# Kernel tuning notes

Measured on AMD Instinct MI355X. Metric: run time of the kernel, lower is better.

The kernel has to match this reference:

```python
import jax, jax.numpy as jnp
import numpy as np

N = 50000
E = 1600000
EP = 500000
D_IN, D_EMB = 64, 32


def setup_inputs() -> dict:
    key = jax.random.key(0)
    ks = jax.random.split(key, 12)
    return {
        "x": jax.random.normal(ks[0], (N, D_IN), dtype=jnp.float32),
        "W1": jax.random.normal(ks[1], (D_IN, D_EMB), dtype=jnp.float32) * (1.0 / np.sqrt(D_IN)),
        "b1": jnp.zeros((D_EMB,), dtype=jnp.float32),
        "W2": jax.random.normal(ks[2], (D_EMB, 2 * D_EMB), dtype=jnp.float32) * (1.0 / np.sqrt(D_EMB)),
        "b2": jnp.zeros((2 * D_EMB,), dtype=jnp.float32),
        "eps": jax.random.normal(ks[3], (N, D_EMB), dtype=jnp.float32),
        "edge_src": jax.random.randint(ks[4], (E,), 0, N, dtype=jnp.int32),
        "edge_dst": jax.random.randint(ks[5], (E,), 0, N, dtype=jnp.int32),
        "pos_src": jax.random.randint(ks[6], (EP,), 0, N, dtype=jnp.int32),
        "pos_dst": jax.random.randint(ks[7], (EP,), 0, N, dtype=jnp.int32),
        "neg_src": jax.random.randint(ks[8], (EP,), 0, N, dtype=jnp.int32),
        "neg_dst": jax.random.randint(ks[9], (EP,), 0, N, dtype=jnp.int32),
    }


def _degree_norms(src, dst, n):
    ones = jnp.ones(src.shape, dtype=jnp.float32)
    out_deg = jax.ops.segment_sum(ones, src, num_segments=n)
    in_deg = jax.ops.segment_sum(ones, dst, num_segments=n)
    # DGL GraphConv norm='both': clamp degrees to >=1, pow(-0.5)
    return jnp.clip(out_deg, 1.0) ** -0.5, jnp.clip(in_deg, 1.0) ** -0.5


def _graph_conv(h, src, dst, norm_src, norm_dst, W, b, n):
    # rst = D_dst^{-1/2} A D_src^{-1/2} h W + b
    msg = (h * norm_src[:, None])[src]                       # [E, d] gather
    agg = jax.ops.segment_sum(msg, dst, num_segments=n)      # [N, d] scatter-add
    return (agg * norm_dst[:, None]) @ W + b


def _dot_predict(z, u, v):
    # u_dot_v: per-edge inner product of endpoint embeddings
    return jnp.sum(z[u] * z[v], axis=-1)


def reference(x, W1, b1, W2, b2, eps, edge_src, edge_dst,
              pos_src, pos_dst, neg_src, neg_dst):
    n = x.shape[0]
    ns, nd = _degree_norms(edge_src, edge_dst, n)
    h = _graph_conv(x, edge_src, edge_dst, ns, nd, W1, b1, n)
    h = jax.nn.relu(h)  # dropout = identity (eval mode)
    h = _graph_conv(h, edge_src, edge_dst, ns, nd, W2, b2, n)
    mu, log_var = jnp.split(h, 2, axis=-1)
    sigma = jnp.exp(log_var / 2.0)
    z = mu + sigma * eps
    pos = _dot_predict(z, pos_src, pos_dst)
    neg = _dot_predict(z, neg_src, neg_dst)
    return pos, neg, mu, sigma
```

## Files before the change

### kernel.cpp

```cpp
#include <hip/hip_runtime.h>
#include <math.h>

#define NN  50000
#define NE  1600000
#define NEP 500000
#define DIN 64
#define DE  32

#define BKT_SH 7
#define NB     391
#define S1B    256
#define CHK    6250
#define HBS    128
#define HCHKS  12500
#define HWRD   12500
#define HWRD2  12512
#define XWB    3126
#define CAP    6144
#define NROW   50016

typedef float f4 __attribute__((ext_vector_type(4)));

__device__ __forceinline__ unsigned f2b(float f) {
    unsigned u = __float_as_uint(f);
    return (u + 0x7FFFu + ((u >> 16) & 1u)) >> 16;
}
__device__ __forceinline__ unsigned pack2(float a, float b) {
    return f2b(a) | (f2b(b) << 16);
}
__device__ __forceinline__ float blo(unsigned u) { return __uint_as_float(u << 16); }
__device__ __forceinline__ float bhi(unsigned u) { return __uint_as_float(u & 0xFFFF0000u); }

__global__ __launch_bounds__(256) void k_hist(const int* __restrict__ src,
                                              const int* __restrict__ dst,
                                              unsigned* __restrict__ partialS,
                                              unsigned* __restrict__ partialD,
                                              int* __restrict__ T) {
    __shared__ unsigned h[HWRD2];
    int t = threadIdx.x;
    int isS = blockIdx.x < HBS;
    int chunk = isS ? blockIdx.x : blockIdx.x - HBS;
    const int* e = isS ? src : dst;
    int chk = isS ? HCHKS : CHK;
    for (int i = t; i < HWRD2; i += 256) h[i] = 0;
    __syncthreads();
    int beg = chunk * chk;
    const int ev = beg + chk;
    int i = beg + t;
    for (; i + 1792 < ev; i += 2048) {
        int s0 = e[i],        s1 = e[i + 256],  s2 = e[i + 512],  s3 = e[i + 768];
        int s4 = e[i + 1024], s5 = e[i + 1280], s6 = e[i + 1536], s7 = e[i + 1792];
        atomicAdd(&h[s0 >> 2], 1u << ((s0 & 3) * 8));
        atomicAdd(&h[s1 >> 2], 1u << ((s1 & 3) * 8));
        atomicAdd(&h[s2 >> 2], 1u << ((s2 & 3) * 8));
        atomicAdd(&h[s3 >> 2], 1u << ((s3 & 3) * 8));
        atomicAdd(&h[s4 >> 2], 1u << ((s4 & 3) * 8));
        atomicAdd(&h[s5 >> 2], 1u << ((s5 & 3) * 8));
        atomicAdd(&h[s6 >> 2], 1u << ((s6 & 3) * 8));
        atomicAdd(&h[s7 >> 2], 1u << ((s7 & 3) * 8));
    }
    for (; i < ev; i += 256) {
        int s = e[i];
        atomicAdd(&h[s >> 2], 1u << ((s & 3) * 8));
    }
    __syncthreads();
    unsigned* pout = (isS ? partialS : partialD) + (size_t)chunk * HWRD;
    for (int i2 = t; i2 < HWRD; i2 += 256) pout[i2] = h[i2];
    if (!isS) {
        for (int c = t; c < NB; c += 256) {
            int sum = 0;
#pragma unroll
            for (int k = 0; k < 32; k++) {
                unsigned v = h[c * 32 + ((k + t) & 31)];
                sum += (int)(v & 0xFFu) + (int)((v >> 8) & 0xFFu)
                     + (int)((v >> 16) & 0xFFu) + (int)(v >> 24);
            }
            T[chunk * NB + c] = sum;
        }
    }
}

__global__ __launch_bounds__(512) void k_s2h(const int* __restrict__ T,
                                             int* __restrict__ Base,
                                             int* __restrict__ BS,
                                             const unsigned* __restrict__ partialS,
                                             const unsigned* __restrict__ partialD,
                                             int* __restrict__ dout,
                                             int* __restrict__ din) {
    int t = threadIdx.x;
    if (blockIdx.x == 0) {
        __shared__ int tot[512];
        int run = 0;
        if (t < NB) {
            for (int b = 0; b < S1B; b += 8) {
                int v0 = T[(b + 0) * NB + t];
                int v1 = T[(b + 1) * NB + t];
                int v2 = T[(b + 2) * NB + t];
                int v3 = T[(b + 3) * NB + t];
                int v4 = T[(b + 4) * NB + t];
                int v5 = T[(b + 5) * NB + t];
                int v6 = T[(b + 6) * NB + t];
                int v7 = T[(b + 7) * NB + t];
                Base[(b + 0) * NB + t] = run; run += v0;
                Base[(b + 1) * NB + t] = run; run += v1;
                Base[(b + 2) * NB + t] = run; run += v2;
                Base[(b + 3) * NB + t] = run; run += v3;
                Base[(b + 4) * NB + t] = run; run += v4;
                Base[(b + 5) * NB + t] = run; run += v5;
                Base[(b + 6) * NB + t] = run; run += v6;
                Base[(b + 7) * NB + t] = run; run += v7;
            }
        }
        tot[t] = (t < NB) ? run : 0;
        __syncthreads();
        for (int off = 1; off < 512; off <<= 1) {
            int v = (t >= off) ? tot[t - off] : 0;
            __syncthreads();
            tot[t] += v;
            __syncthreads();
        }
        if (t < NB) BS[t] = (t == 0) ? 0 : tot[t - 1];
        if (t == 0) BS[NB] = NE;
    } else if (blockIdx.x < 26) {
        int w = (blockIdx.x - 1) * 512 + t;
        if (w < HWRD) {
            int c0 = 0, c1 = 0, c2 = 0, c3 = 0;
#pragma unroll 8
            for (int b = 0; b < HBS; b++) {
                unsigned v = partialS[(size_t)b * HWRD + w];
                c0 += (int)(v & 0xFFu);
                c1 += (int)((v >> 8) & 0xFFu);
                c2 += (int)((v >> 16) & 0xFFu);
                c3 += (int)(v >> 24);
            }
            ((int4*)dout)[w] = make_int4(c0, c1, c2, c3);
        }
    } else {
        int w = (blockIdx.x - 26) * 512 + t;
        if (w < HWRD) {
            int c0 = 0, c1 = 0, c2 = 0, c3 = 0;
#pragma unroll 8
            for (int b = 0; b < S1B; b++) {
                unsigned v = partialD[(size_t)b * HWRD + w];
                c0 += (int)(v & 0xFFu);
                c1 += (int)((v >> 8) & 0xFFu);
                c2 += (int)((v >> 16) & 0xFFu);
                c3 += (int)(v >> 24);
            }
            ((int4*)din)[w] = make_int4(c0, c1, c2, c3);
        }
    }
}

__global__ __launch_bounds__(512) void k_s3(const int* __restrict__ src,
                                            const int* __restrict__ dst,
                                            const int* __restrict__ T,
                                            const int* __restrict__ Base,
                                            const int* __restrict__ BS,
                                            unsigned* __restrict__ tmp) {
    __shared__ int scn[512];
    __shared__ int delta[NB];
    __shared__ int cur[NB];
    __shared__ unsigned buf[CHK];
    int t = threadIdx.x;
    int beg = blockIdx.x * CHK;
    scn[t] = (t < NB) ? T[blockIdx.x * NB + t] : 0;
    __syncthreads();
    for (int off = 1; off < 512; off <<= 1) {
        int v = (t >= off) ? scn[t - off] : 0;
        __syncthreads();
        scn[t] += v;
        __syncthreads();
    }
    if (t < NB) {
        int ls = (t == 0) ? 0 : scn[t - 1];
        cur[t] = ls;
        delta[t] = Base[blockIdx.x * NB + t] + BS[t] - ls;
    }
    __syncthreads();
    {
        const int ev = beg + CHK;
        int i = beg + t;
        for (; i + 1536 < ev; i += 2048) {
            int d0 = dst[i],        s0 = src[i];
            int d1 = dst[i + 512],  s1 = src[i + 512];
            int d2 = dst[i + 1024], s2 = src[i + 1024];
            int d3 = dst[i + 1536], s3 = src[i + 1536];
            int l0 = atomicAdd(&cur[d0 >> BKT_SH], 1); buf[l0] = (unsigned)s0 | ((unsigned)d0 << 16);
            int l1 = atomicAdd(&cur[d1 >> BKT_SH], 1); buf[l1] = (unsigned)s1 | ((unsigned)d1 << 16);
            int l2 = atomicAdd(&cur[d2 >> BKT_SH], 1); buf[l2] = (unsigned)s2 | ((unsigned)d2 << 16);
            int l3 = atomicAdd(&cur[d3 >> BKT_SH], 1); buf[l3] = (unsigned)s3 | ((unsigned)d3 << 16);
        }
        for (; i < ev; i += 512) {
            int d = dst[i];
            int s = src[i];
            int lp = atomicAdd(&cur[d >> BKT_SH], 1);
            buf[lp] = (unsigned)s | ((unsigned)d << 16);
        }
    }
    __syncthreads();
    for (int i = t; i < CHK; i += 512) {
        unsigned e = buf[i];
        tmp[delta[e >> (16 + BKT_SH)] + i] = e;
    }
}

__global__ __launch_bounds__(256) void k_s4x(const unsigned* __restrict__ tmp,
                                             const int* __restrict__ BS,
                                             const int* __restrict__ din,
                                             ushort* __restrict__ csr,
                                             unsigned* __restrict__ prow,
                                             const float* __restrict__ x,
                                             const float* __restrict__ W1,
                                             const int* __restrict__ dout,
                                             unsigned* __restrict__ xw1b) {
    __shared__ float sW[DIN * DE];
    int t = threadIdx.x;
    if (blockIdx.x < NB) {
        int* scn = (int*)sW;
        int* cur = scn + 128;
        int p = blockIdx.x;
        int ebeg = BS[p];
        int ne = BS[p + 1] - ebeg;
        int myd = 0;
        if (t < 128) {
            int node = (p << BKT_SH) + t;
            myd = (node < NN) ? din[node] : 0;
            scn[t] = (myd + 7) & ~7;
        }
        __syncthreads();
        for (int off = 1; off < 128; off <<= 1) {
            int v = 0;
            if (t < 128 && t >= off) v = scn[t - off];
            __syncthreads();
            if (t < 128) scn[t] += v;
            __syncthreads();
        }
        if (t < 128) {
            int ps = p * CAP + scn[t] - ((myd + 7) & ~7);
            cur[t] = ps;
            int node = (p << BKT_SH) + t;
            if (node < NN) prow[node] = (unsigned)ps | ((unsigned)myd << 24);
        }
        __syncthreads();
        {
            int i = t;
            for (; i + 768 < ne; i += 1024) {
                unsigned e0 = tmp[ebeg + i];
                unsigned e1 = tmp[ebeg + i + 256];
                unsigned e2 = tmp[ebeg + i + 512];
                unsigned e3 = tmp[ebeg + i + 768];
                int l0 = atomicAdd(&cur[(e0 >> 16) & 127], 1); csr[l0] = (ushort)(e0 & 0xFFFFu);
                int l1 = atomicAdd(&cur[(e1 >> 16) & 127], 1); csr[l1] = (ushort)(e1 & 0xFFFFu);
                int l2 = atomicAdd(&cur[(e2 >> 16) & 127], 1); csr[l2] = (ushort)(e2 & 0xFFFFu);
                int l3 = atomicAdd(&cur[(e3 >> 16) & 127], 1); csr[l3] = (ushort)(e3 & 0xFFFFu);
            }
            for (; i < ne; i += 256) {
                unsigned e = tmp[ebeg + i];
                int lp = atomicAdd(&cur[(e >> 16) & 127], 1);
                csr[lp] = (ushort)(e & 0xFFFFu);
            }
        }
        __syncthreads();
        if (t < 128) {
            int end = p * CAP + scn[t];
            for (int q = cur[t]; q < end; q++) csr[q] = (ushort)NN;
        }
    } else {
        for (int i = t; i < DIN * DE; i += 256) sW[i] = W1[i];
        __syncthreads();
        int r  = (blockIdx.x - NB) * 16 + (t >> 4);
        int tc = t & 15;
        if (r >= NN) {
            if (r < NROW) xw1b[r * 16 + tc] = 0u;
            return;
        }
        const float* xr = x + (size_t)r * DIN;
        float a0 = 0.f, a1 = 0.f;
#pragma unroll
        for (int k = 0; k < DIN; k++) {
            float v = xr[k];
            a0 += v * sW[k * DE + 2 * tc];
            a1 += v * sW[k * DE + 2 * tc + 1];
        }
        float ns = rsqrtf(fmaxf((float)dout[r], 1.0f));
        xw1b[r * 16 + tc] = pack2(a0 * ns, a1 * ns);
    }
}

__device__ __forceinline__ void acc8(float* a, uint4 w) {
    a[0] += blo(w.x); a[1] += bhi(w.x);
    a[2] += blo(w.y); a[3] += bhi(w.y);
    a[4] += blo(w.z); a[5] += bhi(w.z);
    a[6] += blo(w.w); a[7] += bhi(w.w);
}

__device__ __forceinline__ void gacc(const uint4* __restrict__ msg, uint4 cw, int l, float* a) {
    uint4 w0 = msg[(int)(cw.x & 0xFFFFu) * 4 + l];
    uint4 w1 = msg[(int)(cw.x >> 16)     * 4 + l];
    uint4 w2 = msg[(int)(cw.y & 0xFFFFu) * 4 + l];
    uint4 w3 = msg[(int)(cw.y >> 16)     * 4 + l];
    uint4 w4 = msg[(int)(cw.z & 0xFFFFu) * 4 + l];
    uint4 w5 = msg[(int)(cw.z >> 16)     * 4 + l];
    uint4 w6 = msg[(int)(cw.w & 0xFFFFu) * 4 + l];
    uint4 w7 = msg[(int)(cw.w >> 16)     * 4 + l];
    acc8(a, w0); acc8(a, w1); acc8(a, w2); acc8(a, w3);
    acc8(a, w4); acc8(a, w5); acc8(a, w6); acc8(a, w7);
}

__device__ __forceinline__ void gather_half(const ushort* __restrict__ crow,
                                            const uint4* __restrict__ msg,
                                            int nb, int h, int l, float* a) {
    const uint4* cp = (const uint4*)crow;
    int b = h;
    if (b >= nb) return;
    uint4 cur = cp[b];
    for (b += 2; b < nb; b += 2) {
        uint4 nxt = cp[b];
        gacc(msg, cur, l, a);
        cur = nxt;
    }
    gacc(msg, cur, l, a);
}

__global__ __launch_bounds__(256) void k_g1(const unsigned* __restrict__ prow,
                                            const ushort* __restrict__ csr,
                                            const uint4* __restrict__ msg,
                                            const int* __restrict__ dout,
                                            const float* __restrict__ b1,
                                            uint4* __restrict__ out) {
    int t = blockIdx.x * 256 + threadIdx.x;
    int r = t >> 3;
    int l = t & 3;
    int h = (t >> 2) & 1;
    if (r >= NN) {
        if (h == 0 && r < NROW) out[r * 4 + l] = make_uint4(0, 0, 0, 0);
        return;
    }
    unsigned pr = prow[r];
    int ps = (int)(pr & 0xFFFFFFu);
    int len = (int)(pr >> 24);
    int nb = (len + 7) >> 3;
    float a[8] = {0, 0, 0, 0, 0, 0, 0, 0};
    gather_half(csr + ps, msg, nb, h, l, a);
#pragma unroll
    for (int k = 0; k < 8; k++) a[k] += __shfl_xor(a[k], 4);
    if (h) return;
    float scd = rsqrtf(fmaxf((float)len, 1.0f));
    float scs = rsqrtf(fmaxf((float)dout[r], 1.0f));
    const float4* b14 = (const float4*)b1;
    float4 bb0 = b14[2 * l], bb1 = b14[2 * l + 1];
    float o0 = fmaxf(scd * a[0] + bb0.x, 0.f) * scs;
    float o1 = fmaxf(scd * a[1] + bb0.y, 0.f) * scs;
    float o2 = fmaxf(scd * a[2] + bb0.z, 0.f) * scs;
    float o3 = fmaxf(scd * a[3] + bb0.w, 0.f) * scs;
    float o4 = fmaxf(scd * a[4] + bb1.x, 0.f) * scs;
    float o5 = fmaxf(scd * a[5] + bb1.y, 0.f) * scs;
    float o6 = fmaxf(scd * a[6] + bb1.z, 0.f) * scs;
    float o7 = fmaxf(scd * a[7] + bb1.w, 0.f) * scs;
    out[r * 4 + l] = make_uint4(pack2(o0, o1), pack2(o2, o3), pack2(o4, o5), pack2(o6, o7));
}

__global__ __launch_bounds__(256) void k_g2f(const unsigned* __restrict__ prow,
                                             const ushort* __restrict__ csr,
                                             const uint4* __restrict__ msg,
                                             const float* __restrict__ W2,
                                             const float* __restrict__ b2,
                                             const float* __restrict__ eps,
                                             float* __restrict__ mu,
                                             float* __restrict__ sigma,
                                             unsigned* __restrict__ zb) {
    __shared__ float sW[DE * 64];
    __shared__ float sb[64];
    int t = threadIdx.x;
    for (int i = t; i < DE * 64; i += 256) sW[i] = W2[i];
    if (t < 64) sb[t] = b2[t];
    __syncthreads();
    int g = blockIdx.x * 256 + t;
    int r = g >> 3;
    int l = g & 3;
    int j = g & 7;
    int h = (g >> 2) & 1;
    if (r >= NN) return;
    unsigned pr = prow[r];
    int ps = (int)(pr & 0xFFFFFFu);
    int len = (int)(pr >> 24);
    int nb = (len + 7) >> 3;
    float a[8] = {0, 0, 0, 0, 0, 0, 0, 0};
    gather_half(csr + ps, msg, nb, h, l, a);
#pragma unroll
    for (int k = 0; k < 8; k++) a[k] += __shfl_xor(a[k], 4);
    float scd = rsqrtf(fmaxf((float)len, 1.0f));
#pragma unroll
    for (int k = 0; k < 8; k++) a[k] *= scd;
    int cbase = 8 * j;
    float o3[8];
#pragma unroll
    for (int c = 0; c < 8; c++) o3[c] = sb[cbase + c];
#pragma unroll
    for (int d = 0; d < 4; d++) {
        int kb = 8 * (l ^ d);
#pragma unroll
        for (int k = 0; k < 8; k++) {
            float av = (d == 0) ? a[k] : __shfl_xor(a[k], d);
            const float* wrow = sW + (kb + k) * 64 + cbase;
#pragma unroll
            for (int c = 0; c < 8; c++) o3[c] += av * wrow[c];
        }
    }
    if (j < 4) {
        f4* mp = (f4*)(mu + (size_t)r * DE + cbase);
        f4 m0 = {o3[0], o3[1], o3[2], o3[3]};
        f4 m1 = {o3[4], o3[5], o3[6], o3[7]};
        __builtin_nontemporal_store(m0, mp);
        __builtin_nontemporal_store(m1, mp + 1);
    }
    float muv[8];
#pragma unroll
    for (int c = 0; c < 8; c++) muv[c] = __shfl_xor(o3[c], 4);
    if (j >= 4) {
        int cc = cbase - DE;
        const f4* ep = (const f4*)(eps + (size_t)r * DE + cc);
        f4 e0 = __builtin_nontemporal_load(ep);
        f4 e1 = __builtin_nontemporal_load(ep + 1);
        float ev[8] = {e0.x, e0.y, e0.z, e0.w, e1.x, e1.y, e1.z, e1.w};
        float sgv[8], zv[8];
#pragma unroll
        for (int c = 0; c < 8; c++) {
            sgv[c] = expf(0.5f * o3[c]);
            zv[c]  = muv[c] + sgv[c] * ev[c];
        }
        f4* sp = (f4*)(sigma + (size_t)r * DE + cc);
        f4 s0 = {sgv[0], sgv[1], sgv[2], sgv[3]};
        f4 s1 = {sgv[4], sgv[5], sgv[6], sgv[7]};
        __builtin_nontemporal_store(s0, sp);
        __builtin_nontemporal_store(s1, sp + 1);
        uint4* zp = (uint4*)(zb + (size_t)r * 16 + (j - 4) * 4);
        zp[0] = make_uint4(pack2(zv[0], zv[1]), pack2(zv[2], zv[3]),
                           pack2(zv[4], zv[5]), pack2(zv[6], zv[7]));
    }
}

__global__ __launch_bounds__(256) void k_dot2(const uint4* __restrict__ zb4,
                                              const int* __restrict__ pu,
                                              const int* __restrict__ pv,
                                              const int* __restrict__ nu,
                                              const int* __restrict__ nv,
                                              float* __restrict__ out) {
    int t = blockIdx.x * 256 + threadIdx.x;
    int e = t >> 2;
    int l = t & 3;
    if (e < 2 * NEP) {
        int ee = (e < NEP) ? e : e - NEP;
        const int* uu = (e < NEP) ? pu : nu;
        const int* vv = (e < NEP) ? pv : nv;
        int a = __builtin_nontemporal_load(uu + ee);
        int b = __builtin_nontemporal_load(vv + ee);
        uint4 za = zb4[a * 4 + l];
        uint4 zc = zb4[b * 4 + l];
        float s = blo(za.x) * blo(zc.x) + bhi(za.x) * bhi(zc.x)
                + blo(za.y) * blo(zc.y) + bhi(za.y) * bhi(zc.y)
                + blo(za.z) * blo(zc.z) + bhi(za.z) * bhi(zc.z)
                + blo(za.w) * blo(zc.w) + bhi(za.w) * bhi(zc.w);
        s += __shfl_xor(s, 1);
        s += __shfl_xor(s, 2);
        if (l == 0) __builtin_nontemporal_store(s, out + e);
    }
}

extern "C" void kernel_launch(void* const* d_in, const int* in_sizes, int n_in,
                              void* d_out, int out_size, void* d_ws, size_t ws_size,
                              hipStream_t stream) {
    const float* x    = (const float*)d_in[0];
    const float* W1   = (const float*)d_in[1];
    const float* b1   = (const float*)d_in[2];
    const float* W2   = (const float*)d_in[3];
    const float* b2   = (const float*)d_in[4];
    const float* eps  = (const float*)d_in[5];
    const int*   esrc = (const int*)d_in[6];
    const int*   edst = (const int*)d_in[7];
    const int*   psrc = (const int*)d_in[8];
    const int*   pdst = (const int*)d_in[9];
    const int*   gsrc = (const int*)d_in[10];
    const int*   gdst = (const int*)d_in[11];

    float* out = (float*)d_out;
    float* pos = out;
    float* mu  = out + 2 * NEP;
    float* sg  = out + 2 * NEP + NN * DE;

    int* wi = (int*)d_ws;
    unsigned* prow     = (unsigned*)wi;
    int*      dout_    = wi + 50004;
    int*      din      = wi + 100004;
    int*      T        = wi + 150004;
    int*      Base     = wi + 250100;
    int*      BS       = wi + 350196;
    unsigned* partialS = (unsigned*)(wi + 350592);
    unsigned* tmp      = partialS;
    unsigned* partialD = (unsigned*)(wi + 1950592);
    ushort*   csr      = (ushort*)partialD;
    unsigned* P0       = (unsigned*)(wi + 5150592);
    unsigned* P1       = P0 + 16 * NROW;

    k_hist<<<HBS + S1B, 256, 0, stream>>>(esrc, edst, partialS, partialD, T);
    k_s2h <<<51, 512, 0, stream>>>(T, Base, BS, partialS, partialD, dout_, din);
    k_s3  <<<S1B, 512, 0, stream>>>(esrc, edst, T, Base, BS, tmp);
    k_s4x <<<NB + XWB, 256, 0, stream>>>(tmp, BS, din, csr, prow, x, W1, dout_, P0);
    k_g1  <<<(NROW * 8) / 256, 256, 0, stream>>>(prow, csr, (const uint4*)P0, dout_, b1, (uint4*)P1);
    k_g2f <<<(NN * 8 + 255) / 256, 256, 0, stream>>>(prow, csr, (const uint4*)P1, W2, b2, eps, mu, sg, P0);
    k_dot2<<<(2 * NEP * 4) / 256, 256, 0, stream>>>((const uint4*)P0, psrc, pdst, gsrc, gdst, pos);
}
```

Before: 191.9 us.

## Derive in-degrees from bucketed edges instead of a full destination histogram

The per-node destination histogram (partialD, 256 blocks × 12500 words) and its reduction are removed. Destination blocks now count only per-bucket totals, and each bucket block in k_s4x recounts per-node in-degrees from the bucket-sorted tmp array in shared memory before building its CSR. This cuts a large partial-histogram write and read plus the extra reduction blocks, at the cost of one more pass over tmp per bucket. Block sizes are also doubled across k_hist, k_s3 and k_s4x.

```diff
diff --git a/kernel.cpp b/kernel.cpp
--- a/kernel.cpp
+++ b/kernel.cpp
@@ -14,8 +14,7 @@
 #define HBS    128
 #define HCHKS  12500
 #define HWRD   12500
-#define HWRD2  12512
-#define XWB    3126
+#define XWB    1563
 #define CAP    6144
 #define NROW   50016
 
@@ -31,52 +30,61 @@
 __device__ __forceinline__ float blo(unsigned u) { return __uint_as_float(u << 16); }
 __device__ __forceinline__ float bhi(unsigned u) { return __uint_as_float(u & 0xFFFF0000u); }
 
-__global__ __launch_bounds__(256) void k_hist(const int* __restrict__ src,
+__global__ __launch_bounds__(512) void k_hist(const int* __restrict__ src,
                                               const int* __restrict__ dst,
                                               unsigned* __restrict__ partialS,
-                                              unsigned* __restrict__ partialD,
                                               int* __restrict__ T) {
-    __shared__ unsigned h[HWRD2];
+    __shared__ unsigned h[HWRD];
     int t = threadIdx.x;
-    int isS = blockIdx.x < HBS;
-    int chunk = isS ? blockIdx.x : blockIdx.x - HBS;
-    const int* e = isS ? src : dst;
-    int chk = isS ? HCHKS : CHK;
-    for (int i = t; i < HWRD2; i += 256) h[i] = 0;
-    __syncthreads();
-    int beg = chunk * chk;
-    const int ev = beg + chk;
-    int i = beg + t;
-    for (; i + 1792 < ev; i += 2048) {
-        int s0 = e[i],        s1 = e[i + 256],  s2 = e[i + 512],  s3 = e[i + 768];
-        int s4 = e[i + 1024], s5 = e[i + 1280], s6 = e[i + 1536], s7 = e[i + 1792];
-        atomicAdd(&h[s0 >> 2], 1u << ((s0 & 3) * 8));
-        atomicAdd(&h[s1 >> 2], 1u << ((s1 & 3) * 8));
-        atomicAdd(&h[s2 >> 2], 1u << ((s2 & 3) * 8));
-        atomicAdd(&h[s3 >> 2], 1u << ((s3 & 3) * 8));
-        atomicAdd(&h[s4 >> 2], 1u << ((s4 & 3) * 8));
-        atomicAdd(&h[s5 >> 2], 1u << ((s5 & 3) * 8));
-        atomicAdd(&h[s6 >> 2], 1u << ((s6 & 3) * 8));
-        atomicAdd(&h[s7 >> 2], 1u << ((s7 & 3) * 8));
-    }
-    for (; i < ev; i += 256) {
-        int s = e[i];
-        atomicAdd(&h[s >> 2], 1u << ((s & 3) * 8));
-    }
-    __syncthreads();
-    unsigned* pout = (isS ? partialS : partialD) + (size_t)chunk * HWRD;
-    for (int i2 = t; i2 < HWRD; i2 += 256) pout[i2] = h[i2];
-    if (!isS) {
-        for (int c = t; c < NB; c += 256) {
-            int sum = 0;
-#pragma unroll
-            for (int k = 0; k < 32; k++) {
-                unsigned v = h[c * 32 + ((k + t) & 31)];
-                sum += (int)(v & 0xFFu) + (int)((v >> 8) & 0xFFu)
-                     + (int)((v >> 16) & 0xFFu) + (int)(v >> 24);
-            }
-            T[chunk * NB + c] = sum;
-        }
+    if (blockIdx.x < HBS) {
+        for (int i = t; i < HWRD; i += 512) h[i] = 0;
+        __syncthreads();
+        int beg = blockIdx.x * HCHKS;
+        const int ev = beg + HCHKS;
+        int i = beg + t;
+        for (; i + 3584 < ev; i += 4096) {
+            int s0 = src[i],        s1 = src[i + 512],  s2 = src[i + 1024], s3 = src[i + 1536];
+            int s4 = src[i + 2048], s5 = src[i + 2560], s6 = src[i + 3072], s7 = src[i + 3584];
+            atomicAdd(&h[s0 >> 2], 1u << ((s0 & 3) * 8));
+            atomicAdd(&h[s1 >> 2], 1u << ((s1 & 3) * 8));
+            atomicAdd(&h[s2 >> 2], 1u << ((s2 & 3) * 8));
+            atomicAdd(&h[s3 >> 2], 1u << ((s3 & 3) * 8));
+            atomicAdd(&h[s4 >> 2], 1u << ((s4 & 3) * 8));
+            atomicAdd(&h[s5 >> 2], 1u << ((s5 & 3) * 8));
+            atomicAdd(&h[s6 >> 2], 1u << ((s6 & 3) * 8));
+            atomicAdd(&h[s7 >> 2], 1u << ((s7 & 3) * 8));
+        }
+        for (; i < ev; i += 512) {
+            int s = src[i];
+            atomicAdd(&h[s >> 2], 1u << ((s & 3) * 8));
+        }
+        __syncthreads();
+        unsigned* p = partialS + (size_t)blockIdx.x * HWRD;
+        for (int i2 = t; i2 < HWRD; i2 += 512) p[i2] = h[i2];
+    } else {
+        int b = blockIdx.x - HBS;
+        int* cd = (int*)h;
+        for (int i = t; i < NB; i += 512) cd[i] = 0;
+        __syncthreads();
+        int beg = b * CHK;
+        const int ev = beg + CHK;
+        int i = beg + t;
+        for (; i + 3584 < ev; i += 4096) {
+            int d0 = dst[i],        d1 = dst[i + 512],  d2 = dst[i + 1024], d3 = dst[i + 1536];
+            int d4 = dst[i + 2048], d5 = dst[i + 2560], d6 = dst[i + 3072], d7 = dst[i + 3584];
+            atomicAdd(&cd[d0 >> BKT_SH], 1);
+            atomicAdd(&cd[d1 >> BKT_SH], 1);
+            atomicAdd(&cd[d2 >> BKT_SH], 1);
+            atomicAdd(&cd[d3 >> BKT_SH], 1);
+            atomicAdd(&cd[d4 >> BKT_SH], 1);
+            atomicAdd(&cd[d5 >> BKT_SH], 1);
+            atomicAdd(&cd[d6 >> BKT_SH], 1);
+            atomicAdd(&cd[d7 >> BKT_SH], 1);
+        }
+        for (; i < ev; i += 512)
+            atomicAdd(&cd[dst[i] >> BKT_SH], 1);
+        __syncthreads();
+        for (int i2 = t; i2 < NB; i2 += 512) T[b * NB + i2] = cd[i2];
     }
 }
 
@@ -84,9 +92,7 @@
                                              int* __restrict__ Base,
                                              int* __restrict__ BS,
                                              const unsigned* __restrict__ partialS,
-                                             const unsigned* __restrict__ partialD,
-                                             int* __restrict__ dout,
-                                             int* __restrict__ din) {
+                                             int* __restrict__ dout) {
     int t = threadIdx.x;
     if (blockIdx.x == 0) {
         __shared__ int tot[512];
@@ -121,7 +127,7 @@
         }
         if (t < NB) BS[t] = (t == 0) ? 0 : tot[t - 1];
         if (t == 0) BS[NB] = NE;
-    } else if (blockIdx.x < 26) {
+    } else {
         int w = (blockIdx.x - 1) * 512 + t;
         if (w < HWRD) {
             int c0 = 0, c1 = 0, c2 = 0, c3 = 0;
@@ -135,41 +141,27 @@
             }
             ((int4*)dout)[w] = make_int4(c0, c1, c2, c3);
         }
-    } else {
-        int w = (blockIdx.x - 26) * 512 + t;
-        if (w < HWRD) {
-            int c0 = 0, c1 = 0, c2 = 0, c3 = 0;
-#pragma unroll 8
-            for (int b = 0; b < S1B; b++) {
-                unsigned v = partialD[(size_t)b * HWRD + w];
-                c0 += (int)(v & 0xFFu);
-                c1 += (int)((v >> 8) & 0xFFu);
-                c2 += (int)((v >> 16) & 0xFFu);
-                c3 += (int)(v >> 24);
-            }
-            ((int4*)din)[w] = make_int4(c0, c1, c2, c3);
-        }
-    }
-}
-
-__global__ __launch_bounds__(512) void k_s3(const int* __restrict__ src,
-                                            const int* __restrict__ dst,
-                                            const int* __restrict__ T,
-                                            const int* __restrict__ Base,
-                                            const int* __restrict__ BS,
-                                            unsigned* __restrict__ tmp) {
+    }
+}
+
+__global__ __launch_bounds__(1024) void k_s3(const int* __restrict__ src,
+                                             const int* __restrict__ dst,
+                                             const int* __restrict__ T,
+                                             const int* __restrict__ Base,
+                                             const int* __restrict__ BS,
+                                             unsigned* __restrict__ tmp) {
     __shared__ int scn[512];
     __shared__ int delta[NB];
     __shared__ int cur[NB];
     __shared__ unsigned buf[CHK];
     int t = threadIdx.x;
     int beg = blockIdx.x * CHK;
-    scn[t] = (t < NB) ? T[blockIdx.x * NB + t] : 0;
+    if (t < 512) scn[t] = (t < NB) ? T[blockIdx.x * NB + t] : 0;
     __syncthreads();
     for (int off = 1; off < 512; off <<= 1) {
-        int v = (t >= off) ? scn[t - off] : 0;
-        __syncthreads();
-        scn[t] += v;
+        int v = (t >= off && t < 512) ? scn[t - off] : 0;
+        __syncthreads();
+        if (t < 512) scn[t] += v;
         __syncthreads();
     }
     if (t < NB) {
@@ -181,17 +173,17 @@
     {
         const int ev = beg + CHK;
         int i = beg + t;
-        for (; i + 1536 < ev; i += 2048) {
+        for (; i + 3072 < ev; i += 4096) {
             int d0 = dst[i],        s0 = src[i];
-            int d1 = dst[i + 512],  s1 = src[i + 512];
-            int d2 = dst[i + 1024], s2 = src[i + 1024];
-            int d3 = dst[i + 1536], s3 = src[i + 1536];
+            int d1 = dst[i + 1024], s1 = src[i + 1024];
+            int d2 = dst[i + 2048], s2 = src[i + 2048];
+            int d3 = dst[i + 3072], s3 = src[i + 3072];
             int l0 = atomicAdd(&cur[d0 >> BKT_SH], 1); buf[l0] = (unsigned)s0 | ((unsigned)d0 << 16);
             int l1 = atomicAdd(&cur[d1 >> BKT_SH], 1); buf[l1] = (unsigned)s1 | ((unsigned)d1 << 16);
             int l2 = atomicAdd(&cur[d2 >> BKT_SH], 1); buf[l2] = (unsigned)s2 | ((unsigned)d2 << 16);
             int l3 = atomicAdd(&cur[d3 >> BKT_SH], 1); buf[l3] = (unsigned)s3 | ((unsigned)d3 << 16);
         }
-        for (; i < ev; i += 512) {
+        for (; i < ev; i += 1024) {
             int d = dst[i];
             int s = src[i];
             int lp = atomicAdd(&cur[d >> BKT_SH], 1);
@@ -199,15 +191,14 @@
         }
     }
     __syncthreads();
-    for (int i = t; i < CHK; i += 512) {
+    for (int i = t; i < CHK; i += 1024) {
         unsigned e = buf[i];
         tmp[delta[e >> (16 + BKT_SH)] + i] = e;
     }
 }
 
-__global__ __launch_bounds__(256) void k_s4x(const unsigned* __restrict__ tmp,
+__global__ __launch_bounds__(512) void k_s4x(const unsigned* __restrict__ tmp,
                                              const int* __restrict__ BS,
-                                             const int* __restrict__ din,
                                              ushort* __restrict__ csr,
                                              unsigned* __restrict__ prow,
                                              const float* __restrict__ x,
@@ -217,17 +208,31 @@
     __shared__ float sW[DIN * DE];
     int t = threadIdx.x;
     if (blockIdx.x < NB) {
-        int* scn = (int*)sW;
-        int* cur = scn + 128;
+        int* cnt = (int*)sW;
+        int* scn = cnt + 128;
+        int* cur = cnt + 256;
         int p = blockIdx.x;
         int ebeg = BS[p];
         int ne = BS[p + 1] - ebeg;
-        int myd = 0;
-        if (t < 128) {
-            int node = (p << BKT_SH) + t;
-            myd = (node < NN) ? din[node] : 0;
-            scn[t] = (myd + 7) & ~7;
-        }
+        if (t < 128) cnt[t] = 0;
+        __syncthreads();
+        {
+            int i = t;
+            for (; i + 1536 < ne; i += 2048) {
+                unsigned e0 = tmp[ebeg + i];
+                unsigned e1 = tmp[ebeg + i + 512];
+                unsigned e2 = tmp[ebeg + i + 1024];
+                unsigned e3 = tmp[ebeg + i + 1536];
+                atomicAdd(&cnt[(e0 >> 16) & 127], 1);
+                atomicAdd(&cnt[(e1 >> 16) & 127], 1);
+                atomicAdd(&cnt[(e2 >> 16) & 127], 1);
+                atomicAdd(&cnt[(e3 >> 16) & 127], 1);
+            }
+            for (; i < ne; i += 512)
+                atomicAdd(&cnt[(tmp[ebeg + i] >> 16) & 127], 1);
+        }
+        __syncthreads();
+        if (t < 128) scn[t] = (cnt[t] + 7) & ~7;
         __syncthreads();
         for (int off = 1; off < 128; off <<= 1) {
             int v = 0;
@@ -237,25 +242,26 @@
             __syncthreads();
         }
         if (t < 128) {
-            int ps = p * CAP + scn[t] - ((myd + 7) & ~7);
+            int pad8 = (cnt[t] + 7) & ~7;
+            int ps = p * CAP + scn[t] - pad8;
             cur[t] = ps;
             int node = (p << BKT_SH) + t;
-            if (node < NN) prow[node] = (unsigned)ps | ((unsigned)myd << 24);
+            if (node < NN) prow[node] = (unsigned)ps | ((unsigned)cnt[t] << 24);
         }
         __syncthreads();
         {
             int i = t;
-            for (; i + 768 < ne; i += 1024) {
+            for (; i + 1536 < ne; i += 2048) {
                 unsigned e0 = tmp[ebeg + i];
-                unsigned e1 = tmp[ebeg + i + 256];
-                unsigned e2 = tmp[ebeg + i + 512];
-                unsigned e3 = tmp[ebeg + i + 768];
+                unsigned e1 = tmp[ebeg + i + 512];
+                unsigned e2 = tmp[ebeg + i + 1024];
+                unsigned e3 = tmp[ebeg + i + 1536];
                 int l0 = atomicAdd(&cur[(e0 >> 16) & 127], 1); csr[l0] = (ushort)(e0 & 0xFFFFu);
                 int l1 = atomicAdd(&cur[(e1 >> 16) & 127], 1); csr[l1] = (ushort)(e1 & 0xFFFFu);
                 int l2 = atomicAdd(&cur[(e2 >> 16) & 127], 1); csr[l2] = (ushort)(e2 & 0xFFFFu);
                 int l3 = atomicAdd(&cur[(e3 >> 16) & 127], 1); csr[l3] = (ushort)(e3 & 0xFFFFu);
             }
-            for (; i < ne; i += 256) {
+            for (; i < ne; i += 512) {
                 unsigned e = tmp[ebeg + i];
                 int lp = atomicAdd(&cur[(e >> 16) & 127], 1);
                 csr[lp] = (ushort)(e & 0xFFFFu);
@@ -267,9 +273,9 @@
             for (int q = cur[t]; q < end; q++) csr[q] = (ushort)NN;
         }
     } else {
-        for (int i = t; i < DIN * DE; i += 256) sW[i] = W1[i];
-        __syncthreads();
-        int r  = (blockIdx.x - NB) * 16 + (t >> 4);
+        for (int i = t; i < DIN * DE; i += 512) sW[i] = W1[i];
+        __syncthreads();
+        int r  = (blockIdx.x - NB) * 32 + (t >> 4);
         int tc = t & 15;
         if (r >= NN) {
             if (r < NROW) xw1b[r * 16 + tc] = 0u;
@@ -492,21 +498,19 @@
     int* wi = (int*)d_ws;
     unsigned* prow     = (unsigned*)wi;
     int*      dout_    = wi + 50004;
-    int*      din      = wi + 100004;
-    int*      T        = wi + 150004;
-    int*      Base     = wi + 250100;
-    int*      BS       = wi + 350196;
-    unsigned* partialS = (unsigned*)(wi + 350592);
+    int*      T        = wi + 100004;
+    int*      Base     = wi + 200100;
+    int*      BS       = wi + 300196;
+    unsigned* partialS = (unsigned*)(wi + 300592);
     unsigned* tmp      = partialS;
-    unsigned* partialD = (unsigned*)(wi + 1950592);
-    ushort*   csr      = (ushort*)partialD;
-    unsigned* P0       = (unsigned*)(wi + 5150592);
+    ushort*   csr      = (ushort*)(wi + 1900592);
+    unsigned* P0       = (unsigned*)(wi + 3101760);
     unsigned* P1       = P0 + 16 * NROW;
 
-    k_hist<<<HBS + S1B, 256, 0, stream>>>(esrc, edst, partialS, partialD, T);
-    k_s2h <<<51, 512, 0, stream>>>(T, Base, BS, partialS, partialD, dout_, din);
-    k_s3  <<<S1B, 512, 0, stream>>>(esrc, edst, T, Base, BS, tmp);
-    k_s4x <<<NB + XWB, 256, 0, stream>>>(tmp, BS, din, csr, prow, x, W1, dout_, P0);
+    k_hist<<<HBS + S1B, 512, 0, stream>>>(esrc, edst, partialS, T);
+    k_s2h <<<26, 512, 0, stream>>>(T, Base, BS, partialS, dout_);
+    k_s3  <<<S1B, 1024, 0, stream>>>(esrc, edst, T, Base, BS, tmp);
+    k_s4x <<<NB + XWB, 512, 0, stream>>>(tmp, BS, csr, prow, x, W1, dout_, P0);
     k_g1  <<<(NROW * 8) / 256, 256, 0, stream>>>(prow, csr, (const uint4*)P0, dout_, b1, (uint4*)P1);
     k_g2f <<<(NN * 8 + 255) / 256, 256, 0, stream>>>(prow, csr, (const uint4*)P1, W2, b2, eps, mu, sg, P0);
     k_dot2<<<(2 * NEP * 4) / 256, 256, 0, stream>>>((const uint4*)P0, psrc, pdst, gsrc, gdst, pos);
```

Result: faster. 187.2 us (-2.5%).
